# Performance work log

Hardware: AMD Instinct MI355X
Metric: run time of the kernel (lower is better)

## Reference

```python
import jax, jax.numpy as jnp
import numpy as np

B, T, D, H = 64, 512, 256, 512  # batch, seq_len, embed_dim, enc_units


def _lstm(x_tbd, U, xW, reverse):
    """Keras LSTM with activation='sigmoid' (all gates AND candidate/output use sigmoid).
    x_tbd: [T,B,D] (only for shape), xW: precomputed x@W+b [T,B,4H], U: [H,4H].
    Gate order in Keras kernels: i, f, c(g), o."""
    if reverse:
        xW = xW[::-1]
    b = xW.shape[1]
    h0 = jnp.zeros((b, U.shape[0]), xW.dtype)
    c0 = jnp.zeros((b, U.shape[0]), xW.dtype)

    def step(carry, xw):
        h, c = carry
        z = xw + h @ U  # [B,4H]
        i, f, g, o = jnp.split(z, 4, axis=-1)
        i = jax.nn.sigmoid(i)
        f = jax.nn.sigmoid(f)
        g = jax.nn.sigmoid(g)  # activation='sigmoid' (not tanh)
        o = jax.nn.sigmoid(o)
        c_new = f * c + i * g
        h_new = o * jax.nn.sigmoid(c_new)  # activation='sigmoid' (not tanh)
        return (h_new, c_new), h_new

    (h_last, c_last), hs = jax.lax.scan(step, (h0, c0), xW)
    if reverse:
        hs = hs[::-1]  # Bidirectional re-reverses backward outputs to align in time
    return hs, h_last, c_last


def setup_inputs() -> dict:
    key = jax.random.key(0)
    ks = jax.random.split(key, 6)
    s_in = 1.0 / np.sqrt(D)
    s_rec = 1.0 / np.sqrt(H)
    return {
        "x": jax.random.normal(ks[0], (B, T, D), jnp.float32),
        "hidden": jax.random.normal(ks[1], (2 * B, H), jnp.float32),  # unused by call()
        "Wf": jax.random.normal(ks[2], (D, 4 * H), jnp.float32) * s_in,
        "Uf": jax.random.normal(ks[3], (H, 4 * H), jnp.float32) * s_rec,
        "bf": jnp.zeros((4 * H,), jnp.float32),
        "Wb": jax.random.normal(ks[4], (D, 4 * H), jnp.float32) * s_in,
        "Ub": jax.random.normal(ks[5], (H, 4 * H), jnp.float32) * s_rec,
        "bb": jnp.zeros((4 * H,), jnp.float32),
    }


def reference(x, hidden, Wf, Uf, bf, Wb, Ub, bb):
    x_tbd = jnp.transpose(x, (1, 0, 2))  # [T,B,D]
    # Precompute input projections for all timesteps (hoisted out of the scan)
    xWf = jnp.einsum('tbd,dh->tbh', x_tbd, Wf) + bf
    xWb = jnp.einsum('tbd,dh->tbh', x_tbd, Wb) + bb
    hs_f, hF, cF = _lstm(x_tbd, Uf, xWf, reverse=False)
    hs_b, hB, cB = _lstm(x_tbd, Ub, xWb, reverse=True)
    out = 0.5 * (hs_f + hs_b)  # merge_mode='ave'
    out = jnp.transpose(out, (1, 0, 2))  # [B,T,H]
    return out, hF, cF, hB, cB
```

## Files before the change

kernel.cpp:

```cpp
#include <hip/hip_runtime.h>
#include <hip/hip_bf16.h>
#include <cstdint>
#include <cstddef>

#define BB 64
#define TT 512
#define DD 256
#define HH 512
#define G4 2048

typedef __bf16 bf16x8 __attribute__((ext_vector_type(8)));
typedef __bf16 bf16x4 __attribute__((ext_vector_type(4)));
typedef float  f32x4  __attribute__((ext_vector_type(4)));

__device__ __forceinline__ float sigf(float x) {
  return 1.0f / (1.0f + __expf(-x));
}

__global__ void cvt_x_kernel(const float* __restrict__ x, __bf16* __restrict__ xb) {
  int i = (blockIdx.x * 256 + threadIdx.x) * 4;
  float4 v = *(const float4*)(x + i);
  bf16x4 o;
  o[0] = (__bf16)v.x; o[1] = (__bf16)v.y; o[2] = (__bf16)v.z; o[3] = (__bf16)v.w;
  *(bf16x4*)(xb + i) = o;
}

__launch_bounds__(256, 1)
__global__ void lstm_kernel(const __bf16* __restrict__ xb,
                            const float* __restrict__ Wf, const float* __restrict__ Uf,
                            const float* __restrict__ bf_,
                            const float* __restrict__ Wb, const float* __restrict__ Ub,
                            const float* __restrict__ bb_,
                            __bf16* __restrict__ hbuf,
                            unsigned int* __restrict__ counters,
                            float* __restrict__ out,
                            __bf16* __restrict__ hsb) {
  const int bx  = blockIdx.x;
  const int dir = bx >> 5;
  const int s   = bx & 31;
  const float* Wd = dir ? Wb : Wf;
  const float* Ud = dir ? Ub : Uf;
  const float* bd = dir ? bb_ : bf_;
  unsigned int* cnt = counters + dir * 64;
  __bf16* hb = hbuf + (size_t)dir * 2 * BB * HH;

  const int tid  = threadIdx.x;
  const int mt   = tid >> 6;
  const int lane = tid & 63;
  const int j    = lane & 15;
  const int q    = lane >> 4;
  const int colg = s * 16 + j;

  bf16x8 wfrag[4][24];
#pragma unroll
  for (int g = 0; g < 4; ++g) {
    const int col = g * HH + colg;
#pragma unroll
    for (int kt = 0; kt < 24; ++kt) {
      bf16x8 v;
#pragma unroll
      for (int e = 0; e < 8; ++e) {
        const int k = kt * 32 + q * 8 + e;
        const float w = (k < DD) ? Wd[(size_t)k * G4 + col]
                                 : Ud[(size_t)(k - DD) * G4 + col];
        v[e] = (__bf16)w;
      }
      wfrag[g][kt] = v;
    }
  }
  float bg[4];
#pragma unroll
  for (int g = 0; g < 4; ++g) bg[g] = bd[g * HH + colg];

  float cst[4] = {0.f, 0.f, 0.f, 0.f};
  const size_t outTail = (size_t)BB * TT * HH;

  for (int tau = 0; tau < TT; ++tau) {
    const int t = dir ? (TT - 1 - tau) : tau;

    const __bf16* xrow = xb + ((size_t)(mt * 16 + j) * TT + t) * DD + q * 8;
    f32x4 acc[4];
#pragma unroll
    for (int g = 0; g < 4; ++g) acc[g] = (f32x4){bg[g], bg[g], bg[g], bg[g]};
#pragma unroll
    for (int kt = 0; kt < 8; ++kt) {
      bf16x8 a = *(const bf16x8*)(xrow + kt * 32);
#pragma unroll
      for (int g = 0; g < 4; ++g)
        acc[g] = __builtin_amdgcn_mfma_f32_16x16x32_bf16(a, wfrag[g][kt], acc[g], 0, 0, 0);
    }

    if (tau) {
      if (tid == 0) {
        const unsigned int target = 32u * (unsigned int)tau;
        while (__hip_atomic_load(cnt, __ATOMIC_ACQUIRE, __HIP_MEMORY_SCOPE_AGENT) < target)
          __builtin_amdgcn_s_sleep(2);
      }
      __syncthreads();
    }

    const __bf16* hrow = hb + (size_t)(tau & 1) * (BB * HH) + (size_t)(mt * 16 + j) * HH + q * 8;
#pragma unroll
    for (int kt = 0; kt < 16; ++kt) {
      bf16x8 a = *(const bf16x8*)(hrow + kt * 32);
#pragma unroll
      for (int g = 0; g < 4; ++g)
        acc[g] = __builtin_amdgcn_mfma_f32_16x16x32_bf16(a, wfrag[g][8 + kt], acc[g], 0, 0, 0);
    }

    __bf16* hnext = hb + (size_t)((tau + 1) & 1) * (BB * HH);
#pragma unroll
    for (int r = 0; r < 4; ++r) {
      const float zi = acc[0][r], zf = acc[1][r], zg = acc[2][r], zo = acc[3][r];
      const float gi = sigf(zi), gf = sigf(zf), gg = sigf(zg), go = sigf(zo);
      const float cn = gf * cst[r] + gi * gg;
      cst[r] = cn;
      const float hn = go * sigf(cn);
      const int orow = mt * 16 + q * 4 + r;
      hnext[(size_t)orow * HH + colg] = (__bf16)hn;
      if (dir == 0) {
        out[(size_t)orow * (TT * HH) + (size_t)t * HH + colg] = 0.5f * hn;
      } else {
        hsb[(size_t)t * (BB * HH) + (size_t)orow * HH + colg] = (__bf16)hn;
      }
      if (tau == TT - 1) {
        float* base = out + outTail + (size_t)dir * (2 * BB * HH);
        base[(size_t)orow * HH + colg] = hn;
        base[(size_t)BB * HH + (size_t)orow * HH + colg] = cn;
      }
    }

    __syncthreads();
    if (tid == 0)
      __hip_atomic_fetch_add(cnt, 1u, __ATOMIC_RELEASE, __HIP_MEMORY_SCOPE_AGENT);
  }
}

__global__ void combine_kernel(float* __restrict__ out, const __bf16* __restrict__ hsb) {
  const size_t i = ((size_t)blockIdx.x * 256 + threadIdx.x) * 4;
  const size_t b = i >> 18;
  const size_t t = (i >> 9) & 511;
  const size_t c = i & 511;
  bf16x4 hv = *(const bf16x4*)(hsb + t * (BB * HH) + b * HH + c);
  float4 v = *(float4*)(out + i);
  v.x += 0.5f * (float)hv[0];
  v.y += 0.5f * (float)hv[1];
  v.z += 0.5f * (float)hv[2];
  v.w += 0.5f * (float)hv[3];
  *(float4*)(out + i) = v;
}

extern "C" void kernel_launch(void* const* d_in, const int* in_sizes, int n_in,
                              void* d_out, int out_size, void* d_ws, size_t ws_size,
                              hipStream_t stream) {
  (void)in_sizes; (void)n_in; (void)out_size; (void)ws_size;
  const float* x   = (const float*)d_in[0];
  const float* Wf  = (const float*)d_in[2];
  const float* Uf  = (const float*)d_in[3];
  const float* bf_ = (const float*)d_in[4];
  const float* Wb  = (const float*)d_in[5];
  const float* Ub  = (const float*)d_in[6];
  const float* bb_ = (const float*)d_in[7];
  float* out = (float*)d_out;
  char* ws = (char*)d_ws;

  unsigned int* counters = (unsigned int*)ws;
  __bf16* hbuf = (__bf16*)(ws + 1024);
  __bf16* xb   = (__bf16*)(ws + (1 << 19));
  __bf16* hsb  = (__bf16*)(ws + (1 << 19) + (size_t)BB * TT * DD * 2);

  hipMemsetAsync(ws, 0, 1 << 19, stream);
  cvt_x_kernel<<<dim3((BB * TT * DD) / 1024), dim3(256), 0, stream>>>(x, xb);
  lstm_kernel<<<dim3(64), dim3(256), 0, stream>>>(xb, Wf, Uf, bf_, Wb, Ub, bb_,
                                                  hbuf, counters, out, hsb);
  combine_kernel<<<dim3((BB * TT * HH) / 1024), dim3(256), 0, stream>>>(out, hsb);
}
```

Before: 4.347 ms.

## Replace shared atomic counter barrier with per-block flags polled by all waves

Each block now publishes its step count to its own padded flag slot instead of incrementing one shared counter. Every wave polls all 32 flags with one lane per flag and a wave-wide vote, which drops the tid-0 spin and the block-wide barrier before the recurrent matmul. Stores of h, outputs and final states become nontemporal. This aims to cut inter-block barrier latency on the serial 512-step recurrence, but relies on relaxed polls plus explicit fences being correct, and the nontemporal hidden-state stores could slow the cross-block reads.

```diff
diff --git a/kernel.cpp b/kernel.cpp
--- a/kernel.cpp
+++ b/kernel.cpp
@@ -32,7 +32,7 @@
                             const float* __restrict__ Wb, const float* __restrict__ Ub,
                             const float* __restrict__ bb_,
                             __bf16* __restrict__ hbuf,
-                            unsigned int* __restrict__ counters,
+                            unsigned int* __restrict__ flags,
                             float* __restrict__ out,
                             __bf16* __restrict__ hsb) {
   const int bx  = blockIdx.x;
@@ -41,7 +41,8 @@
   const float* Wd = dir ? Wb : Wf;
   const float* Ud = dir ? Ub : Uf;
   const float* bd = dir ? bb_ : bf_;
-  unsigned int* cnt = counters + dir * 64;
+  unsigned int* flbase = flags + (size_t)dir * 32 * 32;
+  unsigned int* myflag = flbase + (size_t)s * 32;
   __bf16* hb = hbuf + (size_t)dir * 2 * BB * HH;
 
   const int tid  = threadIdx.x;
@@ -74,6 +75,7 @@
 
   float cst[4] = {0.f, 0.f, 0.f, 0.f};
   const size_t outTail = (size_t)BB * TT * HH;
+  unsigned int* pollp = flbase + (size_t)(lane & 31) * 32;
 
   for (int tau = 0; tau < TT; ++tau) {
     const int t = dir ? (TT - 1 - tau) : tau;
@@ -91,12 +93,16 @@
     }
 
     if (tau) {
-      if (tid == 0) {
-        const unsigned int target = 32u * (unsigned int)tau;
-        while (__hip_atomic_load(cnt, __ATOMIC_ACQUIRE, __HIP_MEMORY_SCOPE_AGENT) < target)
-          __builtin_amdgcn_s_sleep(2);
+      const unsigned int target = (unsigned int)tau;
+      int iters = 0;
+      for (;;) {
+        unsigned int v = __hip_atomic_load(pollp, __ATOMIC_RELAXED, __HIP_MEMORY_SCOPE_AGENT);
+        if (__all((int)(v >= target))) break;
+        __builtin_amdgcn_s_sleep(1);
+        if ((++iters & 63) == 63)
+          (void)__hip_atomic_load(pollp, __ATOMIC_ACQUIRE, __HIP_MEMORY_SCOPE_AGENT);
       }
-      __syncthreads();
+      __builtin_amdgcn_fence(__ATOMIC_ACQUIRE, "agent");
     }
 
     const __bf16* hrow = hb + (size_t)(tau & 1) * (BB * HH) + (size_t)(mt * 16 + j) * HH + q * 8;
@@ -117,22 +123,27 @@
       cst[r] = cn;
       const float hn = go * sigf(cn);
       const int orow = mt * 16 + q * 4 + r;
-      hnext[(size_t)orow * HH + colg] = (__bf16)hn;
+      __builtin_nontemporal_store((__bf16)hn, hnext + (size_t)orow * HH + colg);
       if (dir == 0) {
-        out[(size_t)orow * (TT * HH) + (size_t)t * HH + colg] = 0.5f * hn;
+        __builtin_nontemporal_store(0.5f * hn,
+            out + (size_t)orow * (TT * HH) + (size_t)t * HH + colg);
       } else {
-        hsb[(size_t)t * (BB * HH) + (size_t)orow * HH + colg] = (__bf16)hn;
+        __builtin_nontemporal_store((__bf16)hn,
+            hsb + (size_t)t * (BB * HH) + (size_t)orow * HH + colg);
       }
       if (tau == TT - 1) {
         float* base = out + outTail + (size_t)dir * (2 * BB * HH);
-        base[(size_t)orow * HH + colg] = hn;
-        base[(size_t)BB * HH + (size_t)orow * HH + colg] = cn;
+        __builtin_nontemporal_store(hn, base + (size_t)orow * HH + colg);
+        __builtin_nontemporal_store(cn, base + (size_t)BB * HH + (size_t)orow * HH + colg);
       }
     }
 
     __syncthreads();
-    if (tid == 0)
-      __hip_atomic_fetch_add(cnt, 1u, __ATOMIC_RELEASE, __HIP_MEMORY_SCOPE_AGENT);
+    if (tid == 0) {
+      __builtin_amdgcn_fence(__ATOMIC_RELEASE, "agent");
+      __hip_atomic_store(myflag, (unsigned int)(tau + 1), __ATOMIC_RELAXED,
+                         __HIP_MEMORY_SCOPE_AGENT);
+    }
   }
 }
 
@@ -164,14 +175,14 @@
   float* out = (float*)d_out;
   char* ws = (char*)d_ws;
 
-  unsigned int* counters = (unsigned int*)ws;
-  __bf16* hbuf = (__bf16*)(ws + 1024);
+  unsigned int* flags = (unsigned int*)ws;
+  __bf16* hbuf = (__bf16*)(ws + 8192);
   __bf16* xb   = (__bf16*)(ws + (1 << 19));
   __bf16* hsb  = (__bf16*)(ws + (1 << 19) + (size_t)BB * TT * DD * 2);
 
   hipMemsetAsync(ws, 0, 1 << 19, stream);
   cvt_x_kernel<<<dim3((BB * TT * DD) / 1024), dim3(256), 0, stream>>>(x, xb);
   lstm_kernel<<<dim3(64), dim3(256), 0, stream>>>(xb, Wf, Uf, bf_, Wb, Ub, bb_,
-                                                  hbuf, counters, out, hsb);
+                                                  hbuf, flags, out, hsb);
   combine_kernel<<<dim3((BB * TT * HH) / 1024), dim3(256), 0, stream>>>(out, hsb);
 }
```

Result: slower. 4.830 ms (+11.1%).
